# Performance work log

Measured on AMD Instinct MI355X. Metric: run time of the kernel, lower is better.

## Reference

```python
import jax, jax.numpy as jnp
import numpy as np

SINKHORN_ITERS = 10


def _optimal_transport(attn, phi, iters):
    # attn: [N,H,W,W], phi: scalar dustbin score
    bs, h, w, _ = attn.shape
    marginal = jnp.concatenate([jnp.ones((w,), attn.dtype), jnp.array([float(w)], attn.dtype)]) / (2.0 * w)
    log_mu = jnp.log(marginal)  # [W+1], broadcasts over [N,H,W+1]
    log_nu = log_mu
    # augment with dustbin row/col filled with phi -> [N,H,W+1,W+1]
    sim = jnp.concatenate([attn, jnp.broadcast_to(phi, (bs, h, w, 1))], axis=-1)
    sim = jnp.concatenate([sim, jnp.broadcast_to(phi, (bs, h, 1, w + 1))], axis=-2)

    def body(i, uv):
        u, v = uv
        v = log_nu - jax.nn.logsumexp(sim + u[..., :, None], axis=2)
        u = log_mu - jax.nn.logsumexp(sim + v[..., None, :], axis=3)
        return (u, v)

    u0 = jnp.zeros((bs, h, w + 1), attn.dtype)
    u, v = jax.lax.fori_loop(0, iters, body, (u0, u0))
    attn_ot = sim + u[..., :, None] + v[..., None, :]
    return jnp.exp(attn_ot + jnp.log(2.0 * w))


def _compute_low_res_disp(pos_shift, attn, occ_mask=None):
    # attn: [N,H,W,W] (dustbins removed); pos_shift: [W,W]
    w = attn.shape[-1]
    high_response = jnp.argmax(attn, axis=-1)  # [N,H,W]
    response_range = jnp.stack([high_response - 1, high_response, high_response + 1], axis=-1)  # [N,H,W,3]
    attn_pad = jnp.pad(attn, ((0, 0), (0, 0), (0, 0), (1, 1)))
    attn_rw = jnp.take_along_axis(attn_pad, response_range + 1, axis=-1)  # [N,H,W,3]
    norm = attn_rw.sum(-1, keepdims=True)
    norm = jnp.where(norm < 0.1, 1.0, norm)  # occ_mask is None branch
    attn_rw = attn_rw / norm
    pos_pad = jnp.pad(pos_shift, ((0, 0), (1, 1)))  # [W,W+2]
    pos_pad = jnp.broadcast_to(pos_pad[None, None], attn_pad.shape)
    pos_rw = jnp.take_along_axis(pos_pad, response_range + 1, axis=-1)
    disp = (attn_rw * pos_rw).sum(-1)  # [N,H,W]
    return disp, norm


def setup_inputs() -> dict:
    key = jax.random.key(0)
    k1, _ = jax.random.split(key)
    N, H, W = 4, 120, 256
    attn_weight = jax.random.normal(k1, (N, H, W, W), dtype=jnp.float32)
    phi = jnp.zeros((1,), dtype=jnp.float32)
    return {"attn_weight": attn_weight, "phi": phi}


def reference(attn_weight, phi):
    w = attn_weight.shape[2]
    attn_ot = _optimal_transport(attn_weight, phi[0], SINKHORN_ITERS)  # [N,H,W+1,W+1]
    # relative position shift, clamped at 0
    pos = jnp.arange(w, dtype=attn_weight.dtype)
    pos_shift = jnp.maximum(pos[:, None] - pos[None, :], 0.0)  # [W,W]
    disp_pred_low_res, matched_attn = _compute_low_res_disp(pos_shift, attn_ot[..., :-1, :-1], None)
    occ_pred = 1.0 - matched_attn.squeeze(-1)  # [N,H,W]
    return disp_pred_low_res, occ_pred
```

## Files before the change

### kernel.cpp

```cpp
#include <hip/hip_runtime.h>
#include <cstdint>

namespace {

constexpr int W = 256;
constexpr int ITERS = 10;
constexpr int PSTR = 260;
constexpr int NG = 16;

__global__ __launch_bounds__(1024)
void sinkhorn_disp_kernel(
    const float* __restrict__ attn,
    const float* __restrict__ phi_p,
    float* __restrict__ out,
    int nh)
{
  __shared__ __align__(16) float E_lds[1024 * 32];
  __shared__ __align__(16) float fpart[NG][PSTR];
  __shared__ __align__(16) float eu[W + 4];
  __shared__ __align__(16) float ev[W + 4];
  __shared__ __align__(16) float win[W][4];
  __shared__ int   jmax[W];
  __shared__ float Seu_s, Sev_s, ephi_s;

  const int tid = threadIdx.x;
  const int tc  = tid & 31;
  const int tr  = tid >> 5;
  const int bid = blockIdx.x;
  const int sw  = tid & 7;
  float* myE = &E_lds[tid * 32];
  #define RDCH(c) (*(const float4*)&myE[4 * ((c) ^ sw)])

  float Er[4][8];
  {
    const float* src = attn + (size_t)bid * (W * W) + (size_t)(tr * 8) * W + tc * 8;
    #pragma unroll
    for (int a = 0; a < 4; ++a) {
      float4 x0 = *(const float4*)(src + a * W);
      float4 x1 = *(const float4*)(src + a * W + 4);
      Er[a][0] = __expf(x0.x); Er[a][1] = __expf(x0.y);
      Er[a][2] = __expf(x0.z); Er[a][3] = __expf(x0.w);
      Er[a][4] = __expf(x1.x); Er[a][5] = __expf(x1.y);
      Er[a][6] = __expf(x1.z); Er[a][7] = __expf(x1.w);
    }
    #pragma unroll
    for (int ap = 0; ap < 4; ++ap) {
      float4 x0 = *(const float4*)(src + (4 + ap) * W);
      float4 x1 = *(const float4*)(src + (4 + ap) * W + 4);
      float4 e0 = make_float4(__expf(x0.x), __expf(x0.y), __expf(x0.z), __expf(x0.w));
      float4 e1 = make_float4(__expf(x1.x), __expf(x1.y), __expf(x1.z), __expf(x1.w));
      *(float4*)&myE[4 * ((2 * ap)     ^ sw)] = e0;
      *(float4*)&myE[4 * ((2 * ap + 1) ^ sw)] = e1;
    }
  }
  if (tid <= W) eu[tid] = 1.0f;
  if (tid == 0) ephi_s = __expf(phi_p[0]);
  __syncthreads();

  const float inv2w = 1.0f / (2.0f * W);

  for (int it = 0; it < ITERS; ++it) {
    {
      float4 u0 = *(const float4*)&eu[tr * 8];
      float4 u1 = *(const float4*)&eu[tr * 8 + 4];
      float ul[8] = {u0.x, u0.y, u0.z, u0.w, u1.x, u1.y, u1.z, u1.w};
      float cp[8];
      #pragma unroll
      for (int b = 0; b < 8; ++b) cp[b] = 0.0f;
      #pragma unroll
      for (int a = 0; a < 4; ++a) {
        #pragma unroll
        for (int b = 0; b < 8; ++b) cp[b] = __builtin_fmaf(Er[a][b], ul[a], cp[b]);
      }
      #pragma unroll
      for (int ap = 0; ap < 4; ++ap) {
        float4 e0 = RDCH(2 * ap), e1 = RDCH(2 * ap + 1);
        float ua = ul[4 + ap];
        cp[0] = __builtin_fmaf(e0.x, ua, cp[0]);
        cp[1] = __builtin_fmaf(e0.y, ua, cp[1]);
        cp[2] = __builtin_fmaf(e0.z, ua, cp[2]);
        cp[3] = __builtin_fmaf(e0.w, ua, cp[3]);
        cp[4] = __builtin_fmaf(e1.x, ua, cp[4]);
        cp[5] = __builtin_fmaf(e1.y, ua, cp[5]);
        cp[6] = __builtin_fmaf(e1.z, ua, cp[6]);
        cp[7] = __builtin_fmaf(e1.w, ua, cp[7]);
      }
      #pragma unroll
      for (int b = 0; b < 8; ++b) cp[b] += __shfl_xor(cp[b], 32, 64);
      if (!(tr & 1)) {
        float4* dst = (float4*)&fpart[tr >> 1][tc * 8];
        dst[0] = make_float4(cp[0], cp[1], cp[2], cp[3]);
        dst[1] = make_float4(cp[4], cp[5], cp[6], cp[7]);
      }
    }
    if (tid < 64) {
      float s = eu[tid] + eu[tid + 64] + eu[tid + 128] + eu[tid + 192];
      if (tid == 0) s += eu[W];
      #pragma unroll
      for (int off = 32; off > 0; off >>= 1) s += __shfl_xor(s, off, 64);
      if (tid == 0) Seu_s = s;
    }
    __syncthreads();
    if (tid < W) {
      float s = 0.0f;
      #pragma unroll
      for (int g = 0; g < NG; ++g) s += fpart[g][tid];
      s += ephi_s * eu[W];
      ev[tid] = inv2w / s;
    } else if (tid == W) {
      ev[W] = 0.5f / (ephi_s * Seu_s);
    }
    __syncthreads();
    {
      float4 v0 = *(const float4*)&ev[tc * 8];
      float4 v1 = *(const float4*)&ev[tc * 8 + 4];
      float vl[8] = {v0.x, v0.y, v0.z, v0.w, v1.x, v1.y, v1.z, v1.w};
      float rp[8];
      #pragma unroll
      for (int a = 0; a < 8; ++a) rp[a] = 0.0f;
      #pragma unroll
      for (int a = 0; a < 4; ++a) {
        #pragma unroll
        for (int b = 0; b < 8; ++b) rp[a] = __builtin_fmaf(Er[a][b], vl[b], rp[a]);
      }
      #pragma unroll
      for (int ap = 0; ap < 4; ++ap) {
        float4 e0 = RDCH(2 * ap), e1 = RDCH(2 * ap + 1);
        float s = e0.x * vl[0] + e0.y * vl[1] + e0.z * vl[2] + e0.w * vl[3]
                + e1.x * vl[4] + e1.y * vl[5] + e1.z * vl[6] + e1.w * vl[7];
        rp[4 + ap] = s;
      }
      #pragma unroll
      for (int a = 0; a < 8; ++a) rp[a] += __shfl_xor(rp[a], 16, 64);
      if (!(tc & 16)) {
        float4* dst = (float4*)&fpart[tc][tr * 8];
        dst[0] = make_float4(rp[0], rp[1], rp[2], rp[3]);
        dst[1] = make_float4(rp[4], rp[5], rp[6], rp[7]);
      }
    }
    if (tid < 64) {
      float s = ev[tid] + ev[tid + 64] + ev[tid + 128] + ev[tid + 192];
      if (tid == 0) s += ev[W];
      #pragma unroll
      for (int off = 32; off > 0; off >>= 1) s += __shfl_xor(s, off, 64);
      if (tid == 0) Sev_s = s;
    }
    __syncthreads();
    if (tid < W) {
      float s = 0.0f;
      #pragma unroll
      for (int g = 0; g < NG; ++g) s += fpart[g][tid];
      s += ephi_s * ev[W];
      eu[tid] = inv2w / s;
    } else if (tid == W) {
      eu[W] = 0.5f / (ephi_s * Sev_s);
    }
    __syncthreads();
  }

  if (tid < W) { win[tid][0] = 0.0f; win[tid][1] = 0.0f; win[tid][2] = 0.0f; }
  float vl[8];
  {
    float4 v0 = *(const float4*)&ev[tc * 8];
    float4 v1 = *(const float4*)&ev[tc * 8 + 4];
    vl[0] = v0.x; vl[1] = v0.y; vl[2] = v0.z; vl[3] = v0.w;
    vl[4] = v1.x; vl[5] = v1.y; vl[6] = v1.z; vl[7] = v1.w;
  }
  {
    #pragma unroll
    for (int a = 0; a < 8; ++a) {
      float m = -1.0f; int mj = 0;
      if (a < 4) {
        #pragma unroll
        for (int b = 0; b < 8; ++b) {
          float vv = Er[a < 4 ? a : 0][b] * vl[b];
          if (vv > m) { m = vv; mj = tc * 8 + b; }
        }
      } else {
        float4 e0 = RDCH(2 * (a - 4)), e1 = RDCH(2 * (a - 4) + 1);
        float e8[8] = {e0.x, e0.y, e0.z, e0.w, e1.x, e1.y, e1.z, e1.w};
        #pragma unroll
        for (int b = 0; b < 8; ++b) {
          float vv = e8[b] * vl[b];
          if (vv > m) { m = vv; mj = tc * 8 + b; }
        }
      }
      unsigned long long best =
          (((unsigned long long)__float_as_uint(m)) << 32) |
          (unsigned)(65535 - mj);
      #pragma unroll
      for (int off = 16; off > 0; off >>= 1) {
        unsigned long long o = __shfl_xor(best, off, 64);
        best = (o > best) ? o : best;
      }
      if (tc == 0) jmax[tr * 8 + a] = 65535 - (int)(best & 0xffffffffull);
    }
  }
  __syncthreads();
  {
    float4 u0 = *(const float4*)&eu[tr * 8];
    float4 u1 = *(const float4*)&eu[tr * 8 + 4];
    float ul[8] = {u0.x, u0.y, u0.z, u0.w, u1.x, u1.y, u1.z, u1.w};
    #pragma unroll
    for (int a = 0; a < 8; ++a) {
      int i  = tr * 8 + a;
      int jm = jmax[i];
      float e8[8];
      if (a < 4) {
        #pragma unroll
        for (int b = 0; b < 8; ++b) e8[b] = Er[a < 4 ? a : 0][b];
      } else {
        float4 e0 = RDCH(2 * (a - 4)), e1 = RDCH(2 * (a - 4) + 1);
        e8[0] = e0.x; e8[1] = e0.y; e8[2] = e0.z; e8[3] = e0.w;
        e8[4] = e1.x; e8[5] = e1.y; e8[6] = e1.z; e8[7] = e1.w;
      }
      #pragma unroll
      for (int b = 0; b < 8; ++b) {
        int k = (tc * 8 + b) - (jm - 1);
        if (k >= 0 && k < 3) {
          win[i][k] = e8[b] * vl[b] * ul[a] * (2.0f * W);
        }
      }
    }
  }
  __syncthreads();
  if (tid < W) {
    const int i  = tid;
    const int jm = jmax[i];
    float w0 = win[i][0], w1 = win[i][1], w2 = win[i][2];
    float norm0 = w0 + w1 + w2;
    float norm  = (norm0 < 0.1f) ? 1.0f : norm0;
    float p0 = fmaxf((float)(i - (jm - 1)), 0.0f);
    float p1 = fmaxf((float)(i - jm),       0.0f);
    float p2 = fmaxf((float)(i - (jm + 1)), 0.0f);
    float disp = (w0 / norm) * p0 + (w1 / norm) * p1 + (w2 / norm) * p2;
    float occ  = 1.0f - norm;
    out[(size_t)bid * W + i] = disp;
    out[(size_t)nh * W + (size_t)bid * W + i] = occ;
  }
  #undef RDCH
}

}

extern "C" void kernel_launch(void* const* d_in, const int* in_sizes, int n_in,
                              void* d_out, int out_size, void* d_ws, size_t ws_size,
                              hipStream_t stream) {
  (void)n_in; (void)d_ws; (void)ws_size; (void)out_size;
  const float* attn = (const float*)d_in[0];
  const float* phi  = (const float*)d_in[1];
  float* out = (float*)d_out;
  const int nh = in_sizes[0] / (W * W);
  sinkhorn_disp_kernel<<<dim3(nh), dim3(1024), 0, stream>>>(attn, phi, out, nh);
}
```

Baseline: 246.6 us.

## Keep row scalings in registers and drop one barrier per Sinkhorn iteration

The row sums in the second half of each iteration are now fully reduced with wave shuffles, so every thread gets its row scalings directly in registers. This removes the fpart round trip through shared memory and one __syncthreads per iteration. The dustbin scalars are recomputed redundantly in each thread from small double-buffered partial-sum arrays, instead of by a dedicated thread. The per-thread swizzled LDS cache of exp values is replaced by a chunk-major float4 layout. The trade is extra shuffle instructions (a 5-step reduction of 8 values instead of 1 step) and redundant scalar work in exchange for fewer barriers and less LDS traffic.

```diff
diff --git a/kernel.cpp b/kernel.cpp
--- a/kernel.cpp
+++ b/kernel.cpp
@@ -5,8 +5,6 @@
 
 constexpr int W = 256;
 constexpr int ITERS = 10;
-constexpr int PSTR = 260;
-constexpr int NG = 16;
 
 __global__ __launch_bounds__(1024)
 void sinkhorn_disp_kernel(
@@ -15,21 +13,20 @@
     float* __restrict__ out,
     int nh)
 {
-  __shared__ __align__(16) float E_lds[1024 * 32];
-  __shared__ __align__(16) float fpart[NG][PSTR];
-  __shared__ __align__(16) float eu[W + 4];
+  __shared__ __align__(16) float4 Echk[8][1024];
+  __shared__ __align__(16) float fpart[16][260];
   __shared__ __align__(16) float ev[W + 4];
   __shared__ __align__(16) float win[W][4];
   __shared__ int   jmax[W];
-  __shared__ float Seu_s, Sev_s, ephi_s;
+  __shared__ float seu_part[2][16];
+  __shared__ float sev_part[4];
 
   const int tid = threadIdx.x;
   const int tc  = tid & 31;
   const int tr  = tid >> 5;
   const int bid = blockIdx.x;
-  const int sw  = tid & 7;
-  float* myE = &E_lds[tid * 32];
-  #define RDCH(c) (*(const float4*)&myE[4 * ((c) ^ sw)])
+  const float ephi  = __expf(phi_p[0]);
+  const float inv2w = 1.0f / (2.0f * W);
 
   float Er[4][8];
   {
@@ -47,35 +44,33 @@
     for (int ap = 0; ap < 4; ++ap) {
       float4 x0 = *(const float4*)(src + (4 + ap) * W);
       float4 x1 = *(const float4*)(src + (4 + ap) * W + 4);
-      float4 e0 = make_float4(__expf(x0.x), __expf(x0.y), __expf(x0.z), __expf(x0.w));
-      float4 e1 = make_float4(__expf(x1.x), __expf(x1.y), __expf(x1.z), __expf(x1.w));
-      *(float4*)&myE[4 * ((2 * ap)     ^ sw)] = e0;
-      *(float4*)&myE[4 * ((2 * ap + 1) ^ sw)] = e1;
-    }
-  }
-  if (tid <= W) eu[tid] = 1.0f;
-  if (tid == 0) ephi_s = __expf(phi_p[0]);
+      Echk[2 * ap    ][tid] = make_float4(__expf(x0.x), __expf(x0.y), __expf(x0.z), __expf(x0.w));
+      Echk[2 * ap + 1][tid] = make_float4(__expf(x1.x), __expf(x1.y), __expf(x1.z), __expf(x1.w));
+    }
+  }
+  float eul[8];
+  #pragma unroll
+  for (int a = 0; a < 8; ++a) eul[a] = 1.0f;
+  float euW = 1.0f;
+  float evW = 0.0f;
+  if (tid < 16) seu_part[0][tid] = 16.0f;
   __syncthreads();
-
-  const float inv2w = 1.0f / (2.0f * W);
 
   for (int it = 0; it < ITERS; ++it) {
     {
-      float4 u0 = *(const float4*)&eu[tr * 8];
-      float4 u1 = *(const float4*)&eu[tr * 8 + 4];
-      float ul[8] = {u0.x, u0.y, u0.z, u0.w, u1.x, u1.y, u1.z, u1.w};
       float cp[8];
       #pragma unroll
       for (int b = 0; b < 8; ++b) cp[b] = 0.0f;
       #pragma unroll
       for (int a = 0; a < 4; ++a) {
-        #pragma unroll
-        for (int b = 0; b < 8; ++b) cp[b] = __builtin_fmaf(Er[a][b], ul[a], cp[b]);
+        float ua = eul[a];
+        #pragma unroll
+        for (int b = 0; b < 8; ++b) cp[b] = __builtin_fmaf(Er[a][b], ua, cp[b]);
       }
       #pragma unroll
       for (int ap = 0; ap < 4; ++ap) {
-        float4 e0 = RDCH(2 * ap), e1 = RDCH(2 * ap + 1);
-        float ua = ul[4 + ap];
+        float4 e0 = Echk[2 * ap][tid], e1 = Echk[2 * ap + 1][tid];
+        float ua = eul[4 + ap];
         cp[0] = __builtin_fmaf(e0.x, ua, cp[0]);
         cp[1] = __builtin_fmaf(e0.y, ua, cp[1]);
         cp[2] = __builtin_fmaf(e0.z, ua, cp[2]);
@@ -93,22 +88,18 @@
         dst[1] = make_float4(cp[4], cp[5], cp[6], cp[7]);
       }
     }
-    if (tid < 64) {
-      float s = eu[tid] + eu[tid + 64] + eu[tid + 128] + eu[tid + 192];
-      if (tid == 0) s += eu[W];
-      #pragma unroll
-      for (int off = 32; off > 0; off >>= 1) s += __shfl_xor(s, off, 64);
-      if (tid == 0) Seu_s = s;
-    }
     __syncthreads();
     if (tid < W) {
       float s = 0.0f;
       #pragma unroll
-      for (int g = 0; g < NG; ++g) s += fpart[g][tid];
-      s += ephi_s * eu[W];
-      ev[tid] = inv2w / s;
-    } else if (tid == W) {
-      ev[W] = 0.5f / (ephi_s * Seu_s);
+      for (int g = 0; g < 16; ++g) s += fpart[g][tid];
+      s += ephi * euW;
+      float e = inv2w / s;
+      ev[tid] = e;
+      float t = e;
+      #pragma unroll
+      for (int off = 32; off > 0; off >>= 1) t += __shfl_xor(t, off, 64);
+      if ((tid & 63) == 0) sev_part[tid >> 6] = t;
     }
     __syncthreads();
     {
@@ -125,37 +116,28 @@
       }
       #pragma unroll
       for (int ap = 0; ap < 4; ++ap) {
-        float4 e0 = RDCH(2 * ap), e1 = RDCH(2 * ap + 1);
-        float s = e0.x * vl[0] + e0.y * vl[1] + e0.z * vl[2] + e0.w * vl[3]
-                + e1.x * vl[4] + e1.y * vl[5] + e1.z * vl[6] + e1.w * vl[7];
-        rp[4 + ap] = s;
-      }
-      #pragma unroll
-      for (int a = 0; a < 8; ++a) rp[a] += __shfl_xor(rp[a], 16, 64);
-      if (!(tc & 16)) {
-        float4* dst = (float4*)&fpart[tc][tr * 8];
-        dst[0] = make_float4(rp[0], rp[1], rp[2], rp[3]);
-        dst[1] = make_float4(rp[4], rp[5], rp[6], rp[7]);
-      }
-    }
-    if (tid < 64) {
-      float s = ev[tid] + ev[tid + 64] + ev[tid + 128] + ev[tid + 192];
-      if (tid == 0) s += ev[W];
-      #pragma unroll
-      for (int off = 32; off > 0; off >>= 1) s += __shfl_xor(s, off, 64);
-      if (tid == 0) Sev_s = s;
-    }
-    __syncthreads();
-    if (tid < W) {
-      float s = 0.0f;
-      #pragma unroll
-      for (int g = 0; g < NG; ++g) s += fpart[g][tid];
-      s += ephi_s * ev[W];
-      eu[tid] = inv2w / s;
-    } else if (tid == W) {
-      eu[W] = 0.5f / (ephi_s * Sev_s);
-    }
-    __syncthreads();
+        float4 e0 = Echk[2 * ap][tid], e1 = Echk[2 * ap + 1][tid];
+        rp[4 + ap] = e0.x * vl[0] + e0.y * vl[1] + e0.z * vl[2] + e0.w * vl[3]
+                   + e1.x * vl[4] + e1.y * vl[5] + e1.z * vl[6] + e1.w * vl[7];
+      }
+      #pragma unroll
+      for (int a = 0; a < 8; ++a) {
+        #pragma unroll
+        for (int off = 16; off > 0; off >>= 1) rp[a] += __shfl_xor(rp[a], off, 64);
+      }
+      float seu_r = 0.0f;
+      #pragma unroll
+      for (int g = 0; g < 16; ++g) seu_r += seu_part[it & 1][g];
+      evW = 0.5f / (ephi * (seu_r + euW));
+      float sev_r = sev_part[0] + sev_part[1] + sev_part[2] + sev_part[3];
+      euW = 0.5f / (ephi * (sev_r + evW));
+      float dust = ephi * evW;
+      #pragma unroll
+      for (int a = 0; a < 8; ++a) eul[a] = inv2w / (rp[a] + dust);
+      float s = eul[0] + eul[1] + eul[2] + eul[3] + eul[4] + eul[5] + eul[6] + eul[7];
+      s += __shfl_xor(s, 32, 64);
+      if ((tid & 63) == 0) seu_part[(it + 1) & 1][tid >> 6] = s;
+    }
   }
 
   if (tid < W) { win[tid][0] = 0.0f; win[tid][1] = 0.0f; win[tid][2] = 0.0f; }
@@ -170,20 +152,19 @@
     #pragma unroll
     for (int a = 0; a < 8; ++a) {
       float m = -1.0f; int mj = 0;
+      float e8[8];
       if (a < 4) {
         #pragma unroll
-        for (int b = 0; b < 8; ++b) {
-          float vv = Er[a < 4 ? a : 0][b] * vl[b];
-          if (vv > m) { m = vv; mj = tc * 8 + b; }
-        }
+        for (int b = 0; b < 8; ++b) e8[b] = Er[a < 4 ? a : 0][b];
       } else {
-        float4 e0 = RDCH(2 * (a - 4)), e1 = RDCH(2 * (a - 4) + 1);
-        float e8[8] = {e0.x, e0.y, e0.z, e0.w, e1.x, e1.y, e1.z, e1.w};
-        #pragma unroll
-        for (int b = 0; b < 8; ++b) {
-          float vv = e8[b] * vl[b];
-          if (vv > m) { m = vv; mj = tc * 8 + b; }
-        }
+        float4 e0 = Echk[2 * (a - 4)][tid], e1 = Echk[2 * (a - 4) + 1][tid];
+        e8[0] = e0.x; e8[1] = e0.y; e8[2] = e0.z; e8[3] = e0.w;
+        e8[4] = e1.x; e8[5] = e1.y; e8[6] = e1.z; e8[7] = e1.w;
+      }
+      #pragma unroll
+      for (int b = 0; b < 8; ++b) {
+        float vv = e8[b] * vl[b];
+        if (vv > m) { m = vv; mj = tc * 8 + b; }
       }
       unsigned long long best =
           (((unsigned long long)__float_as_uint(m)) << 32) |
@@ -198,9 +179,6 @@
   }
   __syncthreads();
   {
-    float4 u0 = *(const float4*)&eu[tr * 8];
-    float4 u1 = *(const float4*)&eu[tr * 8 + 4];
-    float ul[8] = {u0.x, u0.y, u0.z, u0.w, u1.x, u1.y, u1.z, u1.w};
     #pragma unroll
     for (int a = 0; a < 8; ++a) {
       int i  = tr * 8 + a;
@@ -210,7 +188,7 @@
         #pragma unroll
         for (int b = 0; b < 8; ++b) e8[b] = Er[a < 4 ? a : 0][b];
       } else {
-        float4 e0 = RDCH(2 * (a - 4)), e1 = RDCH(2 * (a - 4) + 1);
+        float4 e0 = Echk[2 * (a - 4)][tid], e1 = Echk[2 * (a - 4) + 1][tid];
         e8[0] = e0.x; e8[1] = e0.y; e8[2] = e0.z; e8[3] = e0.w;
         e8[4] = e1.x; e8[5] = e1.y; e8[6] = e1.z; e8[7] = e1.w;
       }
@@ -218,7 +196,7 @@
       for (int b = 0; b < 8; ++b) {
         int k = (tc * 8 + b) - (jm - 1);
         if (k >= 0 && k < 3) {
-          win[i][k] = e8[b] * vl[b] * ul[a] * (2.0f * W);
+          win[i][k] = e8[b] * vl[b] * eul[a] * (2.0f * W);
         }
       }
     }
@@ -238,7 +216,6 @@
     out[(size_t)bid * W + i] = disp;
     out[(size_t)nh * W + (size_t)bid * W + i] = occ;
   }
-  #undef RDCH
 }
 
 }
```

New measurement: 266.4 us. 8.0% more time.
